# Kernel optimization log

Hardware: AMD Instinct MI355X
Metric: run time of the kernel (lower is better)

## Reference

```python
import jax, jax.numpy as jnp
import numpy as np

B, CIN, COUT, COFF, H, W = 4, 256, 256, 256, 64, 64
DG, K = 16, 3            # deformable groups, kernel size
KK = K * K               # 9 taps


def _conv3x3(x, w, b):
    y = jax.lax.conv_general_dilated(x, w, window_strides=(1, 1), padding='SAME',
                                     dimension_numbers=('NCHW', 'OIHW', 'NCHW'))
    return y + b[None, :, None, None]


def _bilinear_sample(xg, ys, xs):
    # xg: [B,DG,Cg,H,W]; ys,xs: [B,DG,Ho,Wo] float sampling coords (zero padding outside)
    Bn, dg, Cg, Hh, Ww = xg.shape
    xf = xg.reshape(Bn, dg, Cg, Hh * Ww)
    y0 = jnp.floor(ys)
    x0 = jnp.floor(xs)
    wy = (ys - y0)[:, :, None]  # [B,DG,1,Ho,Wo]
    wx = (xs - x0)[:, :, None]

    def gather(yi, xi):
        valid = (yi >= 0) & (yi < Hh) & (xi >= 0) & (xi < Ww)
        yc = jnp.clip(yi, 0, Hh - 1).astype(jnp.int32)
        xc = jnp.clip(xi, 0, Ww - 1).astype(jnp.int32)
        idx = (yc * Ww + xc).reshape(Bn, dg, 1, -1)
        v = jnp.take_along_axis(xf, jnp.broadcast_to(idx, (Bn, dg, Cg, idx.shape[-1])), axis=-1)
        v = v.reshape(Bn, dg, Cg, ys.shape[2], ys.shape[3])
        return v * valid[:, :, None].astype(xg.dtype)

    v00 = gather(y0, x0)
    v01 = gather(y0, x0 + 1)
    v10 = gather(y0 + 1, x0)
    v11 = gather(y0 + 1, x0 + 1)
    return v00 * (1 - wy) * (1 - wx) + v01 * (1 - wy) * wx + v10 * wy * (1 - wx) + v11 * wy * wx


def _deform_conv2d(x, offset, mask, weight, bias):
    # torchvision modulated deform_conv2d, stride=1, padding=1, dilation=1, groups=1
    Bn, C, Hh, Ww = x.shape
    Cg = C // DG
    xg = x.reshape(Bn, DG, Cg, Hh, Ww)
    # offset channel layout: 2*(g*KK + k) -> dy, +1 -> dx
    off = offset.reshape(Bn, DG, KK, 2, Hh, Ww)
    msk = mask.reshape(Bn, DG, KK, Hh, Ww)
    wk = weight.reshape(weight.shape[0], DG, Cg, K, K)
    hb = jnp.arange(Hh, dtype=x.dtype)[:, None]
    wb = jnp.arange(Ww, dtype=x.dtype)[None, :]
    acc = jnp.zeros((Bn, weight.shape[0], Hh, Ww), dtype=x.dtype)
    for ki in range(K):
        for kj in range(K):
            k = ki * K + kj
            ys = hb - 1 + ki + off[:, :, k, 0]   # padding=1, dilation=1
            xs = wb - 1 + kj + off[:, :, k, 1]
            s = _bilinear_sample(xg, ys, xs) * msk[:, :, k][:, :, None]  # [B,DG,Cg,H,W]
            acc = acc + jnp.einsum('bgchw,ogc->bohw', s, wk[:, :, :, ki, kj])
    return acc + bias[None, :, None, None]


def setup_inputs() -> dict:
    key = jax.random.key(0)
    ks = jax.random.split(key, 10)
    s = 0.02
    return {
        'x': jax.random.normal(ks[0], (B, CIN, H, W), jnp.float32),
        'offset_feat': jax.random.normal(ks[1], (B, COFF, H, W), jnp.float32),
        'weight': jax.random.normal(ks[2], (COUT, CIN, K, K), jnp.float32) * s,
        'bias': jax.random.normal(ks[3], (COUT,), jnp.float32) * s,
        'w1': jax.random.normal(ks[4], (COUT, COFF, K, K), jnp.float32) * s,
        'b1': jax.random.normal(ks[5], (COUT,), jnp.float32) * s,
        'w2': jax.random.normal(ks[6], (COUT, COUT, K, K), jnp.float32) * s,
        'b2': jax.random.normal(ks[7], (COUT,), jnp.float32) * s,
        'w3': jax.random.normal(ks[8], (27 * DG, COUT, K, K), jnp.float32) * 0.01,
        'b3': jax.random.normal(ks[9], (27 * DG,), jnp.float32) * 0.01,
    }


def reference(x, offset_feat, weight, bias, w1, b1, w2, b2, w3, b3):
    out = jax.nn.silu(_conv3x3(offset_feat, w1, b1))
    out = jax.nn.silu(_conv3x3(out, w2, b2))
    out = _conv3x3(out, w3, b3)                 # [B, 27*DG, H, W]
    o1, o2, m = jnp.split(out, 3, axis=1)
    offset = jnp.concatenate([o1, o2], axis=1)  # [B, 2*DG*9, H, W]
    mask = jax.nn.sigmoid(m)                    # [B, DG*9, H, W]
    return _deform_conv2d(x, offset, mask, weight, bias)
```

## Files before the change

### kernel.cpp

```cpp
#include <hip/hip_runtime.h>
#include <math.h>

typedef __attribute__((ext_vector_type(8))) short  bf16x8;
typedef __attribute__((ext_vector_type(8))) unsigned short u16x8;
typedef __attribute__((ext_vector_type(4))) float  f32x4;

#define MTOT 16384

__device__ __forceinline__ float b2f(unsigned short h) {
  return __uint_as_float(((unsigned int)h) << 16);
}
__device__ __forceinline__ unsigned short f2bf(float f) {
  unsigned int u = __float_as_uint(f);
  unsigned int r = (u + 0x7fffu + ((u >> 16) & 1u)) >> 16;
  return (unsigned short)r;
}
__device__ __forceinline__ void gload16(const unsigned short* g, unsigned short* l) {
  __builtin_amdgcn_global_load_lds(
      (const __attribute__((address_space(1))) void*)g,
      (__attribute__((address_space(3))) void*)l, 16, 0, 0);
}

__global__ __launch_bounds__(256) void nhwc_kernel(const float* __restrict__ in,
                                                   unsigned short* __restrict__ out) {
  const int y = blockIdx.x, b = blockIdx.y;
  const int t = threadIdx.x;
  __shared__ float lds[64 * 65];
  for (int c0 = 0; c0 < 256; c0 += 64) {
    #pragma unroll
    for (int i = 0; i < 16; ++i) {
      int cl = i * 4 + (t >> 6);
      int xx = t & 63;
      lds[cl * 65 + xx] = in[(((size_t)b * 256 + c0 + cl) * 64 + y) * 64 + xx];
    }
    __syncthreads();
    const int plane = c0 >> 6;
    #pragma unroll
    for (int i = 0; i < 16; ++i) {
      int xx = i * 4 + (t >> 6);
      int cl = t & 63;
      int m  = (b << 12) + (y << 6) + xx;
      out[((size_t)plane * MTOT + m) * 64 + cl] = f2bf(lds[cl * 65 + xx]);
    }
    __syncthreads();
  }
}

__global__ __launch_bounds__(256) void wprep_kernel(const float* __restrict__ w,
                                                    unsigned short* __restrict__ Wp,
                                                    int NPAD, int COUT_valid) {
  const int kkc4 = blockIdx.x;
  const int kk = kkc4 >> 2, c4 = kkc4 & 3;
  const int co = blockIdx.y * 4 + (threadIdx.x >> 6);
  const int c16 = threadIdx.x & 63;
  float v = (co < COUT_valid) ? w[((size_t)co * 256 + c4 * 64 + c16) * 9 + kk] : 0.0f;
  Wp[((size_t)kkc4 * NPAD + co) * 64 + c16] = f2bf(v);
}

__global__ __launch_bounds__(256) void sampler_kernel(const float* __restrict__ t3,
                                                      const unsigned short* __restrict__ xh,
                                                      unsigned short* __restrict__ S) {
  const int t = threadIdx.x;
  const int g = t & 15;
  const int m = blockIdx.x * 16 + (t >> 4);
  const int b = m >> 12, pix = m & 4095, y = pix >> 6, x = pix & 63;
  const float* off = t3 + (size_t)m * 432;
  const size_t gbase = ((size_t)(g >> 2) * MTOT + ((size_t)b << 12)) * 64 + (g & 3) * 16;

  #pragma unroll
  for (int kk = 0; kk < 9; ++kk) {
    const int ki = kk / 3, kj = kk % 3;
    float dyv = off[2 * (g * 9 + kk)];
    float dxv = off[2 * (g * 9 + kk) + 1];
    float ml  = off[288 + g * 9 + kk];
    float mk  = 1.0f / (1.0f + __expf(-ml));
    float ysf = (float)(y - 1 + ki) + dyv;
    float xsf = (float)(x - 1 + kj) + dxv;
    float y0f = floorf(ysf), x0f = floorf(xsf);
    float wy = ysf - y0f, wx = xsf - x0f;
    int yi0 = (int)y0f, xi0 = (int)x0f;
    int yi1 = yi0 + 1, xi1 = xi0 + 1;
    bool vy0 = (yi0 >= 0) && (yi0 < 64), vy1 = (yi1 >= 0) && (yi1 < 64);
    bool vx0 = (xi0 >= 0) && (xi0 < 64), vx1 = (xi1 >= 0) && (xi1 < 64);
    int yc0 = min(max(yi0, 0), 63), yc1 = min(max(yi1, 0), 63);
    int xc0 = min(max(xi0, 0), 63), xc1 = min(max(xi1, 0), 63);
    float w00 = (vy0 && vx0) ? (1.f - wy) * (1.f - wx) * mk : 0.f;
    float w01 = (vy0 && vx1) ? (1.f - wy) * wx * mk : 0.f;
    float w10 = (vy1 && vx0) ? wy * (1.f - wx) * mk : 0.f;
    float w11 = (vy1 && vx1) ? wy * wx * mk : 0.f;

    float sacc[16];
    #pragma unroll
    for (int c = 0; c < 16; ++c) sacc[c] = 0.f;

    const int p00 = yc0 * 64 + xc0, p01 = yc0 * 64 + xc1;
    const int p10 = yc1 * 64 + xc0, p11 = yc1 * 64 + xc1;
    {
      u16x8 lo = *(const u16x8*)(xh + gbase + (size_t)p00 * 64);
      u16x8 hi = *(const u16x8*)(xh + gbase + (size_t)p00 * 64 + 8);
      #pragma unroll
      for (int j = 0; j < 8; ++j) { sacc[j] += w00 * b2f(lo[j]); sacc[8 + j] += w00 * b2f(hi[j]); }
    }
    {
      u16x8 lo = *(const u16x8*)(xh + gbase + (size_t)p01 * 64);
      u16x8 hi = *(const u16x8*)(xh + gbase + (size_t)p01 * 64 + 8);
      #pragma unroll
      for (int j = 0; j < 8; ++j) { sacc[j] += w01 * b2f(lo[j]); sacc[8 + j] += w01 * b2f(hi[j]); }
    }
    {
      u16x8 lo = *(const u16x8*)(xh + gbase + (size_t)p10 * 64);
      u16x8 hi = *(const u16x8*)(xh + gbase + (size_t)p10 * 64 + 8);
      #pragma unroll
      for (int j = 0; j < 8; ++j) { sacc[j] += w10 * b2f(lo[j]); sacc[8 + j] += w10 * b2f(hi[j]); }
    }
    {
      u16x8 lo = *(const u16x8*)(xh + gbase + (size_t)p11 * 64);
      u16x8 hi = *(const u16x8*)(xh + gbase + (size_t)p11 * 64 + 8);
      #pragma unroll
      for (int j = 0; j < 8; ++j) { sacc[j] += w11 * b2f(lo[j]); sacc[8 + j] += w11 * b2f(hi[j]); }
    }
    u16x8 olo, ohi;
    #pragma unroll
    for (int j = 0; j < 8; ++j) { olo[j] = f2bf(sacc[j]); ohi[j] = f2bf(sacc[8 + j]); }
    unsigned short* sp = S + ((size_t)(kk * 4 + (g >> 2)) * MTOT + m) * 64 + (g & 3) * 16;
    *(u16x8*)sp = olo;
    *(u16x8*)(sp + 8) = ohi;
  }
}

template<int NPAD, int EPI, bool IMPLICIT>
__global__ __launch_bounds__(256, 2) void gemm_kernel(
    const unsigned short* __restrict__ A,
    const unsigned short* __restrict__ W,
    const float* __restrict__ bias,
    void* __restrict__ outp,
    const unsigned short* __restrict__ zbuf,
    int Nvalid) {
  constexpr int BM = 128, BN = 128, BK = 64;
  constexpr int NSTEP = 36;
  constexpr int BUFE = (BM + BN) * BK;
  __shared__ unsigned short lds[2][BUFE];

  const int t = threadIdx.x, lane = t & 63, w = t >> 6;
  const int wm = w >> 1, wn = w & 1;
  const int m0 = blockIdx.x * BM, n0 = blockIdx.y * BN;

  const unsigned short* baseA[4];
  const unsigned short* zsrcA[4];
  unsigned int vmaskA[4];
  #pragma unroll
  for (int i = 0; i < 4; ++i) {
    int c   = (i * 4 + w) * 64 + lane;
    int row = c >> 3;
    int ccl = (c & 7) ^ (row & 7);
    int m   = m0 + row;
    baseA[i] = A + (size_t)m * 64 + ccl * 8;
    zsrcA[i] = zbuf + ccl * 8;
    if (IMPLICIT) {
      int y = (m >> 6) & 63, x = m & 63;
      unsigned int vm = 0;
      #pragma unroll
      for (int kk = 0; kk < 9; ++kk) {
        int dy = kk / 3 - 1, dx = kk % 3 - 1;
        if ((unsigned)(y + dy) < 64u && (unsigned)(x + dx) < 64u) vm |= (1u << kk);
      }
      vmaskA[i] = vm;
    } else {
      vmaskA[i] = 0;
    }
  }
  const unsigned short* baseB[4];
  #pragma unroll
  for (int j = 0; j < 4; ++j) {
    int c   = (j * 4 + w) * 64 + lane;
    int row = c >> 3;
    int ccl = (c & 7) ^ (row & 7);
    baseB[j] = W + (size_t)(n0 + row) * 64 + ccl * 8;
  }

  int offA[4][2], offB[4][2];
  #pragma unroll
  for (int mi = 0; mi < 4; ++mi) {
    int r = wm * 64 + mi * 16 + (lane & 15);
    #pragma unroll
    for (int kh = 0; kh < 2; ++kh) {
      int ccl = kh * 4 + (lane >> 4);
      offA[mi][kh] = r * 64 + ((ccl ^ (r & 7)) * 8);
    }
  }
  #pragma unroll
  for (int nj = 0; nj < 4; ++nj) {
    int r = wn * 64 + nj * 16 + (lane & 15);
    #pragma unroll
    for (int kh = 0; kh < 2; ++kh) {
      int ccl = kh * 4 + (lane >> 4);
      offB[nj][kh] = BM * BK + r * 64 + ((ccl ^ (r & 7)) * 8);
    }
  }

  f32x4 acc[4][4];
  #pragma unroll
  for (int mi = 0; mi < 4; ++mi)
    #pragma unroll
    for (int nj = 0; nj < 4; ++nj) acc[mi][nj] = (f32x4){0.f, 0.f, 0.f, 0.f};

  auto STAGE = [&](int sn, unsigned short* buf) {
    const long boff = (long)sn * (NPAD * 64);
    if (IMPLICIT) {
      int kkn = sn >> 2;
      int q3  = kkn / 3;
      int dy = q3 - 1, dx = kkn - q3 * 3 - 1;
      const long aoff = (long)(sn & 3) * (MTOT * 64) + (long)(dy * 64 + dx) * 64;
      #pragma unroll
      for (int i = 0; i < 4; ++i) {
        const unsigned short* src = ((vmaskA[i] >> kkn) & 1u) ? baseA[i] + aoff : zsrcA[i];
        gload16(src, buf + (i * 4 + w) * 512);
      }
    } else {
      const long aoff = (long)sn * (MTOT * 64);
      #pragma unroll
      for (int i = 0; i < 4; ++i)
        gload16(baseA[i] + aoff, buf + (i * 4 + w) * 512);
    }
    #pragma unroll
    for (int j = 0; j < 4; ++j)
      gload16(baseB[j] + boff, buf + BM * BK + (j * 4 + w) * 512);
  };

  STAGE(0, lds[0]);

  for (int s = 0; s < NSTEP; ++s) {
    if (s + 1 < NSTEP) {
      STAGE(s + 1, lds[(s + 1) & 1]);
      asm volatile("s_waitcnt vmcnt(8)" ::: "memory");
    } else {
      asm volatile("s_waitcnt vmcnt(0)" ::: "memory");
    }
    __builtin_amdgcn_s_barrier();
    __builtin_amdgcn_sched_barrier(0);

    const unsigned short* cb = lds[s & 1];
    bf16x8 af[4][2], bfg[4][2];
    #pragma unroll
    for (int mi = 0; mi < 4; ++mi)
      #pragma unroll
      for (int kh = 0; kh < 2; ++kh)
        af[mi][kh] = *(const bf16x8*)&cb[offA[mi][kh]];
    #pragma unroll
    for (int nj = 0; nj < 4; ++nj)
      #pragma unroll
      for (int kh = 0; kh < 2; ++kh)
        bfg[nj][kh] = *(const bf16x8*)&cb[offB[nj][kh]];

    #pragma unroll
    for (int kh = 0; kh < 2; ++kh)
      #pragma unroll
      for (int mi = 0; mi < 4; ++mi)
        #pragma unroll
        for (int nj = 0; nj < 4; ++nj)
          acc[mi][nj] = __builtin_amdgcn_mfma_f32_16x16x32_bf16(af[mi][kh], bfg[nj][kh],
                                                                acc[mi][nj], 0, 0, 0);
    __builtin_amdgcn_sched_barrier(0);
    asm volatile("s_waitcnt lgkmcnt(0)" ::: "memory");
    __builtin_amdgcn_s_barrier();
  }

  const int gmBase = m0 + wm * 64 + (lane >> 4) * 4;
  const int gnBase = n0 + wn * 64 + (lane & 15);
  #pragma unroll
  for (int nj = 0; nj < 4; ++nj) {
    const int gn = gnBase + nj * 16;
    const float bv = (gn < Nvalid) ? bias[gn] : 0.f;
    #pragma unroll
    for (int mi = 0; mi < 4; ++mi) {
      #pragma unroll
      for (int r = 0; r < 4; ++r) {
        const int gm = gmBase + mi * 16 + r;
        float v = acc[mi][nj][r] + bv;
        if (EPI == 0) {
          float sv = v / (1.0f + __expf(-v));
          ((unsigned short*)outp)[((size_t)(gn >> 6) * MTOT + gm) * 64 + (gn & 63)] = f2bf(sv);
        } else if (EPI == 1) {
          if (gn < Nvalid) ((float*)outp)[(size_t)gm * 432 + gn] = v;
        } else {
          ((float*)outp)[((size_t)(gm >> 12) * 256 + gn) * 4096 + (gm & 4095)] = v;
        }
      }
    }
  }
}

extern "C" void kernel_launch(void* const* d_in, const int* in_sizes, int n_in,
                              void* d_out, int out_size, void* d_ws, size_t ws_size,
                              hipStream_t stream) {
  const float* x      = (const float*)d_in[0];
  const float* offeat = (const float*)d_in[1];
  const float* weight = (const float*)d_in[2];
  const float* bias   = (const float*)d_in[3];
  const float* w1     = (const float*)d_in[4];
  const float* b1     = (const float*)d_in[5];
  const float* w2     = (const float*)d_in[6];
  const float* b2     = (const float*)d_in[7];
  const float* w3     = (const float*)d_in[8];
  const float* b3     = (const float*)d_in[9];
  float* out = (float*)d_out;

  char* ws = (char*)d_ws;
  unsigned short* xh  = (unsigned short*)(ws + 0);
  float*          t3  = (float*)(ws + 8388608);
  unsigned short* Wd  = (unsigned short*)(ws + 36700160);
  unsigned short* zb  = (unsigned short*)(ws + 37879808);
  unsigned short* S   = (unsigned short*)(ws + 37880064);
  unsigned short* fh  = (unsigned short*)(ws + 37880064);
  unsigned short* t1  = (unsigned short*)(ws + 46268672);
  unsigned short* t2  = (unsigned short*)(ws + 54657280);
  unsigned short* W1p = (unsigned short*)(ws + 63045888);
  unsigned short* W2p = (unsigned short*)(ws + 64225536);
  unsigned short* W3p = (unsigned short*)(ws + 65405184);

  hipMemsetAsync(zb, 0, 256, stream);

  nhwc_kernel<<<dim3(64, 4), 256, 0, stream>>>(x, xh);
  nhwc_kernel<<<dim3(64, 4), 256, 0, stream>>>(offeat, fh);
  wprep_kernel<<<dim3(36, 64), 256, 0, stream>>>(w1, W1p, 256, 256);
  wprep_kernel<<<dim3(36, 64), 256, 0, stream>>>(w2, W2p, 256, 256);
  wprep_kernel<<<dim3(36, 128), 256, 0, stream>>>(w3, W3p, 512, 432);
  wprep_kernel<<<dim3(36, 64), 256, 0, stream>>>(weight, Wd, 256, 256);

  gemm_kernel<256, 0, true><<<dim3(128, 2), 256, 0, stream>>>(fh, W1p, b1, t1, zb, 256);
  gemm_kernel<256, 0, true><<<dim3(128, 2), 256, 0, stream>>>(t1, W2p, b2, t2, zb, 256);
  gemm_kernel<512, 1, true><<<dim3(128, 4), 256, 0, stream>>>(t2, W3p, b3, t3, zb, 432);

  sampler_kernel<<<dim3(1024), 256, 0, stream>>>(t3, xh, S);
  gemm_kernel<256, 2, false><<<dim3(128, 2), 256, 0, stream>>>(S, Wd, bias, out, zb, 256);
}
```

Baseline: 201.0 us.

## Use 8-wave blocks for SiLU convs and split-K with atomics for later GEMMs

Moves the first two implicit-GEMM convolutions to a 512-thread, 8-wave block so each wave holds a smaller 64x32 output tile. The offset-conv GEMM and the final deform GEMM now split the 36 K-steps across two blocks in z, which zero their outputs with memsets and accumulate into them with float atomics. The aim is to fill more of the GPU with only 256 to 512 tiles per GEMM. In exchange it adds memset passes, atomic write traffic, and a summation order that is not deterministic.

```diff
diff --git a/kernel.cpp b/kernel.cpp
--- a/kernel.cpp
+++ b/kernel.cpp
@@ -128,22 +128,166 @@
   }
 }
 
-template<int NPAD, int EPI, bool IMPLICIT>
-__global__ __launch_bounds__(256, 2) void gemm_kernel(
+__global__ __launch_bounds__(512, 1) void gemm8w_kernel(
     const unsigned short* __restrict__ A,
     const unsigned short* __restrict__ W,
     const float* __restrict__ bias,
-    void* __restrict__ outp,
-    const unsigned short* __restrict__ zbuf,
-    int Nvalid) {
+    unsigned short* __restrict__ outp,
+    const unsigned short* __restrict__ zbuf) {
   constexpr int BM = 128, BN = 128, BK = 64;
   constexpr int NSTEP = 36;
   constexpr int BUFE = (BM + BN) * BK;
   __shared__ unsigned short lds[2][BUFE];
 
   const int t = threadIdx.x, lane = t & 63, w = t >> 6;
+  const int wm = w >> 2, wn = w & 3;
+  const int m0 = blockIdx.x * BM, n0 = blockIdx.y * BN;
+
+  const unsigned short* baseA[2];
+  const unsigned short* zsrcA[2];
+  unsigned int vmaskA[2];
+  #pragma unroll
+  for (int i = 0; i < 2; ++i) {
+    int c   = (i * 8 + w) * 64 + lane;
+    int row = c >> 3;
+    int ccl = (c & 7) ^ (row & 7);
+    int m   = m0 + row;
+    baseA[i] = A + (size_t)m * 64 + ccl * 8;
+    zsrcA[i] = zbuf + ccl * 8;
+    int y = (m >> 6) & 63, x = m & 63;
+    unsigned int vm = 0;
+    #pragma unroll
+    for (int kk = 0; kk < 9; ++kk) {
+      int dy = kk / 3 - 1, dx = kk % 3 - 1;
+      if ((unsigned)(y + dy) < 64u && (unsigned)(x + dx) < 64u) vm |= (1u << kk);
+    }
+    vmaskA[i] = vm;
+  }
+  const unsigned short* baseB[2];
+  #pragma unroll
+  for (int j = 0; j < 2; ++j) {
+    int c   = (j * 8 + w) * 64 + lane;
+    int row = c >> 3;
+    int ccl = (c & 7) ^ (row & 7);
+    baseB[j] = W + (size_t)(n0 + row) * 64 + ccl * 8;
+  }
+
+  int offA[4][2], offB[2][2];
+  #pragma unroll
+  for (int mi = 0; mi < 4; ++mi) {
+    int r = wm * 64 + mi * 16 + (lane & 15);
+    #pragma unroll
+    for (int kh = 0; kh < 2; ++kh) {
+      int ccl = kh * 4 + (lane >> 4);
+      offA[mi][kh] = r * 64 + ((ccl ^ (r & 7)) * 8);
+    }
+  }
+  #pragma unroll
+  for (int nj = 0; nj < 2; ++nj) {
+    int r = wn * 32 + nj * 16 + (lane & 15);
+    #pragma unroll
+    for (int kh = 0; kh < 2; ++kh) {
+      int ccl = kh * 4 + (lane >> 4);
+      offB[nj][kh] = BM * BK + r * 64 + ((ccl ^ (r & 7)) * 8);
+    }
+  }
+
+  f32x4 acc[4][2];
+  #pragma unroll
+  for (int mi = 0; mi < 4; ++mi)
+    #pragma unroll
+    for (int nj = 0; nj < 2; ++nj) acc[mi][nj] = (f32x4){0.f, 0.f, 0.f, 0.f};
+
+  auto STAGE = [&](int sn, unsigned short* buf) {
+    int kkn = sn >> 2;
+    int q3  = kkn / 3;
+    int dy = q3 - 1, dx = kkn - q3 * 3 - 1;
+    const long aoff = (long)(sn & 3) * (MTOT * 64) + (long)(dy * 64 + dx) * 64;
+    const long boff = (long)sn * (256 * 64);
+    #pragma unroll
+    for (int i = 0; i < 2; ++i) {
+      const unsigned short* src = ((vmaskA[i] >> kkn) & 1u) ? baseA[i] + aoff : zsrcA[i];
+      gload16(src, buf + (i * 8 + w) * 512);
+    }
+    #pragma unroll
+    for (int j = 0; j < 2; ++j)
+      gload16(baseB[j] + boff, buf + BM * BK + (j * 8 + w) * 512);
+  };
+
+  STAGE(0, lds[0]);
+
+  for (int s = 0; s < NSTEP; ++s) {
+    if (s + 1 < NSTEP) {
+      STAGE(s + 1, lds[(s + 1) & 1]);
+      asm volatile("s_waitcnt vmcnt(4)" ::: "memory");
+    } else {
+      asm volatile("s_waitcnt vmcnt(0)" ::: "memory");
+    }
+    __builtin_amdgcn_s_barrier();
+    __builtin_amdgcn_sched_barrier(0);
+
+    const unsigned short* cb = lds[s & 1];
+    bf16x8 af[4][2], bfg[2][2];
+    #pragma unroll
+    for (int mi = 0; mi < 4; ++mi)
+      #pragma unroll
+      for (int kh = 0; kh < 2; ++kh)
+        af[mi][kh] = *(const bf16x8*)&cb[offA[mi][kh]];
+    #pragma unroll
+    for (int nj = 0; nj < 2; ++nj)
+      #pragma unroll
+      for (int kh = 0; kh < 2; ++kh)
+        bfg[nj][kh] = *(const bf16x8*)&cb[offB[nj][kh]];
+
+    #pragma unroll
+    for (int kh = 0; kh < 2; ++kh)
+      #pragma unroll
+      for (int mi = 0; mi < 4; ++mi)
+        #pragma unroll
+        for (int nj = 0; nj < 2; ++nj)
+          acc[mi][nj] = __builtin_amdgcn_mfma_f32_16x16x32_bf16(af[mi][kh], bfg[nj][kh],
+                                                                acc[mi][nj], 0, 0, 0);
+    __builtin_amdgcn_sched_barrier(0);
+    asm volatile("s_waitcnt lgkmcnt(0)" ::: "memory");
+    __builtin_amdgcn_s_barrier();
+  }
+
+  const int gmBase = m0 + wm * 64 + (lane >> 4) * 4;
+  const int gnBase = n0 + wn * 32 + (lane & 15);
+  #pragma unroll
+  for (int nj = 0; nj < 2; ++nj) {
+    const int gn = gnBase + nj * 16;
+    const float bv = bias[gn];
+    #pragma unroll
+    for (int mi = 0; mi < 4; ++mi) {
+      #pragma unroll
+      for (int r = 0; r < 4; ++r) {
+        const int gm = gmBase + mi * 16 + r;
+        float v = acc[mi][nj][r] + bv;
+        float sv = v / (1.0f + __expf(-v));
+        outp[((size_t)(gn >> 6) * MTOT + gm) * 64 + (gn & 63)] = f2bf(sv);
+      }
+    }
+  }
+}
+
+template<int NPAD, int EPI, bool IMPLICIT>
+__global__ __launch_bounds__(256, 2) void gemmsk_kernel(
+    const unsigned short* __restrict__ A,
+    const unsigned short* __restrict__ W,
+    const float* __restrict__ bias,
+    float* __restrict__ outp,
+    const unsigned short* __restrict__ zbuf,
+    int Nvalid) {
+  constexpr int BM = 128, BN = 128, BK = 64;
+  constexpr int NSTEP = 18;
+  constexpr int BUFE = (BM + BN) * BK;
+  __shared__ unsigned short lds[2][BUFE];
+
+  const int t = threadIdx.x, lane = t & 63, w = t >> 6;
   const int wm = w >> 1, wn = w & 1;
   const int m0 = blockIdx.x * BM, n0 = blockIdx.y * BN;
+  const int ks0 = blockIdx.z * NSTEP;
 
   const unsigned short* baseA[4];
   const unsigned short* zsrcA[4];
@@ -205,19 +349,20 @@
     for (int nj = 0; nj < 4; ++nj) acc[mi][nj] = (f32x4){0.f, 0.f, 0.f, 0.f};
 
   auto STAGE = [&](int sn, unsigned short* buf) {
-    const long boff = (long)sn * (NPAD * 64);
+    const int gs = ks0 + sn;
+    const long boff = (long)gs * (NPAD * 64);
     if (IMPLICIT) {
-      int kkn = sn >> 2;
+      int kkn = gs >> 2;
       int q3  = kkn / 3;
       int dy = q3 - 1, dx = kkn - q3 * 3 - 1;
-      const long aoff = (long)(sn & 3) * (MTOT * 64) + (long)(dy * 64 + dx) * 64;
+      const long aoff = (long)(gs & 3) * (MTOT * 64) + (long)(dy * 64 + dx) * 64;
       #pragma unroll
       for (int i = 0; i < 4; ++i) {
         const unsigned short* src = ((vmaskA[i] >> kkn) & 1u) ? baseA[i] + aoff : zsrcA[i];
         gload16(src, buf + (i * 4 + w) * 512);
       }
     } else {
-      const long aoff = (long)sn * (MTOT * 64);
+      const long aoff = (long)gs * (MTOT * 64);
       #pragma unroll
       for (int i = 0; i < 4; ++i)
         gload16(baseA[i] + aoff, buf + (i * 4 + w) * 512);
@@ -267,23 +412,21 @@
 
   const int gmBase = m0 + wm * 64 + (lane >> 4) * 4;
   const int gnBase = n0 + wn * 64 + (lane & 15);
+  const bool addb = (ks0 == 0);
   #pragma unroll
   for (int nj = 0; nj < 4; ++nj) {
     const int gn = gnBase + nj * 16;
-    const float bv = (gn < Nvalid) ? bias[gn] : 0.f;
+    const float bv = (addb && gn < Nvalid) ? bias[gn] : 0.f;
     #pragma unroll
     for (int mi = 0; mi < 4; ++mi) {
       #pragma unroll
       for (int r = 0; r < 4; ++r) {
         const int gm = gmBase + mi * 16 + r;
         float v = acc[mi][nj][r] + bv;
-        if (EPI == 0) {
-          float sv = v / (1.0f + __expf(-v));
-          ((unsigned short*)outp)[((size_t)(gn >> 6) * MTOT + gm) * 64 + (gn & 63)] = f2bf(sv);
-        } else if (EPI == 1) {
-          if (gn < Nvalid) ((float*)outp)[(size_t)gm * 432 + gn] = v;
+        if (EPI == 1) {
+          if (gn < Nvalid) unsafeAtomicAdd(&outp[(size_t)gm * 432 + gn], v);
         } else {
-          ((float*)outp)[((size_t)(gm >> 12) * 256 + gn) * 4096 + (gm & 4095)] = v;
+          unsafeAtomicAdd(&outp[((size_t)(gm >> 12) * 256 + gn) * 4096 + (gm & 4095)], v);
         }
       }
     }
@@ -327,10 +470,14 @@
   wprep_kernel<<<dim3(36, 128), 256, 0, stream>>>(w3, W3p, 512, 432);
   wprep_kernel<<<dim3(36, 64), 256, 0, stream>>>(weight, Wd, 256, 256);
 
-  gemm_kernel<256, 0, true><<<dim3(128, 2), 256, 0, stream>>>(fh, W1p, b1, t1, zb, 256);
-  gemm_kernel<256, 0, true><<<dim3(128, 2), 256, 0, stream>>>(t1, W2p, b2, t2, zb, 256);
-  gemm_kernel<512, 1, true><<<dim3(128, 4), 256, 0, stream>>>(t2, W3p, b3, t3, zb, 432);
+  gemm8w_kernel<<<dim3(128, 2), 512, 0, stream>>>(fh, W1p, b1, t1, zb);
+  gemm8w_kernel<<<dim3(128, 2), 512, 0, stream>>>(t1, W2p, b2, t2, zb);
+
+  hipMemsetAsync(t3, 0, 28311552, stream);
+  gemmsk_kernel<512, 1, true><<<dim3(128, 4, 2), 256, 0, stream>>>(t2, W3p, b3, t3, zb, 432);
 
   sampler_kernel<<<dim3(1024), 256, 0, stream>>>(t3, xh, S);
-  gemm_kernel<256, 2, false><<<dim3(128, 2), 256, 0, stream>>>(S, Wd, bias, out, zb, 256);
-}
+
+  hipMemsetAsync(out, 0, (size_t)out_size * 4, stream);
+  gemmsk_kernel<256, 2, false><<<dim3(128, 2, 2), 256, 0, stream>>>(S, Wd, bias, out, zb, 256);
+}
```

Result: slower. 327.1 us, median of 2 (+62.8%).
